# Performance work log

Hardware: AMD Instinct MI355X
Metric: run time of the kernel (lower is better)

The kernel has to match this reference:

```python
import jax, jax.numpy as jnp
import numpy as np
import math

EMB = 1024
HEADS = 16
B, S = 2, 2048


def setup_inputs() -> dict:
    key = jax.random.key(0)
    k_x, k_wq, k_bq, k_wu, k_bu = jax.random.split(key, 5)
    lim = 1.0 / math.sqrt(EMB)
    x = jax.random.normal(k_x, (B, S, EMB), dtype=jnp.float32)
    # nn.Linear weights: [out, in], uniform(-lim, lim)
    wq = jax.random.uniform(k_wq, (EMB, EMB), jnp.float32, -lim, lim)
    bq = jax.random.uniform(k_bq, (EMB,), jnp.float32, -lim, lim)
    wu = jax.random.uniform(k_wu, (EMB, EMB), jnp.float32, -lim, lim)
    bu = jax.random.uniform(k_bu, (EMB,), jnp.float32, -lim, lim)
    return {"x": x, "wq": wq, "bq": bq, "wu": wu, "bu": bu}


def reference(x, wq, bq, wu, bu):
    b, s, emb = x.shape
    hd = emb // HEADS
    # NOTE: faithful to the original bug — Q, K, V all come from toqueries
    q = jnp.einsum('bse,oe->bso', x, wq) + bq  # [B,S,emb]
    # faithful (buggy) reshape: heads in LEADING dim
    qh = q.reshape(HEADS, b, s, hd)
    kh = qh
    vh = qh
    scale = 1.0 / math.sqrt(emb)  # faithful: sqrt(emb), not sqrt(hd)
    scores = jnp.einsum('hbqd,hbkd->hbqk', qh, kh) * scale  # [H,B,S,S]
    attn = jax.nn.softmax(scores, axis=-1)
    out = jnp.einsum('hbqk,hbkd->hbqd', attn, vh)  # [H,B,S,hd]
    out = out.reshape(b, s, emb)
    return jnp.einsum('bse,oe->bso', out, wu) + bu
```

## Files before the change

kernel.cpp:

```cpp
#include <hip/hip_runtime.h>
#include <stdint.h>

#define EMB 1024
#define HEADS 16
#define NB 2
#define NS 2048
#define HD 64
#define NTOK (NB*NS)
#define KVBLK 64
#define QW 32
#define QBLK 128
#define SEXP2 0.04508421676368185f

typedef __attribute__((ext_vector_type(8))) short short8;
typedef __attribute__((ext_vector_type(4))) float f32x4;

__device__ inline unsigned short f2bf(float f) {
  unsigned int x = __builtin_bit_cast(unsigned int, f);
  x += 0x7FFFu + ((x >> 16) & 1u);
  return (unsigned short)(x >> 16);
}

__device__ inline unsigned cvt_pk_bf16(float lo, float hi) {
  unsigned d;
  asm("v_cvt_pk_bf16_f32 %0, %1, %2" : "=v"(d) : "v"(lo), "v"(hi));
  return d;
}

__device__ inline void gld16(const void* g, void* l) {
  __builtin_amdgcn_global_load_lds(
      (const __attribute__((address_space(1))) unsigned int*)g,
      (__attribute__((address_space(3))) unsigned int*)l, 16, 0, 0);
}

__global__ void cvt_bf16_kernel(const float* __restrict__ s,
                                unsigned short* __restrict__ d, int n) {
  int i = (blockIdx.x * blockDim.x + threadIdx.x) * 8;
  if (i >= n) return;
  float4 v0 = *reinterpret_cast<const float4*>(s + i);
  float4 v1 = *reinterpret_cast<const float4*>(s + i + 4);
  short8 o;
  o[0] = (short)f2bf(v0.x); o[1] = (short)f2bf(v0.y);
  o[2] = (short)f2bf(v0.z); o[3] = (short)f2bf(v0.w);
  o[4] = (short)f2bf(v1.x); o[5] = (short)f2bf(v1.y);
  o[6] = (short)f2bf(v1.z); o[7] = (short)f2bf(v1.w);
  *reinterpret_cast<short8*>(d + i) = o;
}

__global__ __launch_bounds__(256) void transpose_kernel(
    const unsigned short* __restrict__ src, unsigned short* __restrict__ dst) {
  __shared__ unsigned short t[64][72];
  const int slab = blockIdx.y, kt = blockIdx.x;
  const unsigned short* s = src + ((size_t)slab * NS + kt * 64) * HD;
  unsigned short* d = dst + (size_t)slab * HD * NS + kt * 64;
  const int tid = threadIdx.x;
  #pragma unroll
  for (int c = 0; c < 2; ++c) {
    int idx = c * 256 + tid;
    int row = idx >> 3, col = (idx & 7) * 8;
    short8 v = *reinterpret_cast<const short8*>(s + row * HD + col);
    *reinterpret_cast<short8*>(&t[row][col]) = v;
  }
  __syncthreads();
  #pragma unroll
  for (int c = 0; c < 2; ++c) {
    int idx = c * 256 + tid;
    int drow = idx >> 3, col = (idx & 7) * 8;
    short8 v;
    #pragma unroll
    for (int j = 0; j < 8; ++j) {
      int p = col + j;
      v[j] = t[(p & 3) * 16 + (p >> 2)][drow];
    }
    *reinterpret_cast<short8*>(d + (size_t)drow * NS + col) = v;
  }
}

template<bool OUT_BF16>
__global__ __launch_bounds__(256) void gemm_bt_kernel(
    const unsigned short* __restrict__ A,
    const unsigned short* __restrict__ Bw,
    const float* __restrict__ bias,
    void* __restrict__ Cout,
    unsigned short* __restrict__ Qscaled,
    int M, int N, int K) {
  __shared__ __align__(16) unsigned short As[2][64 * 64];
  __shared__ __align__(16) unsigned short Bs[2][128 * 64];
  const int tid = threadIdx.x;
  const int lane = tid & 63;
  const int wave = tid >> 6;
  const int wr = wave >> 1, wc = wave & 1;
  const int g = lane >> 4, r = lane & 15;
  const int brow = blockIdx.y * 64;
  const int bcol = blockIdx.x * 128;

  const f32x4 zf = {0.f, 0.f, 0.f, 0.f};
  f32x4 acc[2][4];
  #pragma unroll
  for (int m = 0; m < 2; ++m)
    #pragma unroll
    for (int n = 0; n < 4; ++n) acc[m][n] = zf;

  auto stage = [&](int bb, int k0) {
    #pragma unroll
    for (int i = 0; i < 2; ++i) {
      int base = i * 4096 + wave * 1024;
      int L = base + lane * 16;
      int row = L >> 7, lsl = ((L >> 4) & 7) ^ (row & 7);
      gld16((const char*)A + ((size_t)(brow + row) * K + k0) * 2 + lsl * 16,
            (char*)&As[bb][0] + base);
    }
    #pragma unroll
    for (int i = 0; i < 4; ++i) {
      int base = i * 4096 + wave * 1024;
      int L = base + lane * 16;
      int row = L >> 7, lsl = ((L >> 4) & 7) ^ (row & 7);
      gld16((const char*)Bw + ((size_t)(bcol + row) * K + k0) * 2 + lsl * 16,
            (char*)&Bs[bb][0] + base);
    }
  };

  stage(0, 0);
  int cur = 0;
  for (int k0 = 0; k0 < K; k0 += 64) {
    __syncthreads();
    if (k0 + 64 < K) stage(cur ^ 1, k0 + 64);
    const char* Ac = (const char*)&As[cur][0];
    const char* Bc = (const char*)&Bs[cur][0];
    short8 af[2][2], bfr[4][2];
    #pragma unroll
    for (int m = 0; m < 2; ++m) {
      int row = wr * 32 + m * 16 + r;
      #pragma unroll
      for (int kk = 0; kk < 2; ++kk)
        af[m][kk] = *reinterpret_cast<const short8*>(
            Ac + row * 128 + ((kk * 64 + g * 16) ^ ((row & 7) << 4)));
    }
    #pragma unroll
    for (int n = 0; n < 4; ++n) {
      int row = wc * 64 + n * 16 + r;
      #pragma unroll
      for (int kk = 0; kk < 2; ++kk)
        bfr[n][kk] = *reinterpret_cast<const short8*>(
            Bc + row * 128 + ((kk * 64 + g * 16) ^ ((row & 7) << 4)));
    }
    #pragma unroll
    for (int kk = 0; kk < 2; ++kk)
      #pragma unroll
      for (int m = 0; m < 2; ++m)
        #pragma unroll
        for (int n = 0; n < 4; ++n)
          acc[m][n] = __builtin_amdgcn_mfma_f32_16x16x32_bf16(af[m][kk], bfr[n][kk], acc[m][n], 0, 0, 0);
    cur ^= 1;
  }

  #pragma unroll
  for (int n = 0; n < 4; ++n) {
    int col = bcol + wc * 64 + n * 16 + r;
    float bv = bias[col];
    #pragma unroll
    for (int m = 0; m < 2; ++m) {
      #pragma unroll
      for (int reg = 0; reg < 4; ++reg) {
        int row = brow + wr * 32 + m * 16 + g * 4 + reg;
        float v = acc[m][n][reg] + bv;
        if (OUT_BF16)
          ((unsigned short*)Cout)[(size_t)row * N + col] = f2bf(v);
        else
          ((float*)Cout)[(size_t)row * N + col] = v;
        if (Qscaled)
          Qscaled[(size_t)row * N + col] = f2bf(v * SEXP2);
      }
    }
  }
}

__global__ __launch_bounds__(256) void attn_kernel(
    const unsigned short* __restrict__ qb,
    const unsigned short* __restrict__ qsb,
    const unsigned short* __restrict__ vtb,
    unsigned short* __restrict__ ob) {
  const int slab = blockIdx.y;
  const int qtile = blockIdx.x;
  const unsigned short* Qs = qb + (size_t)slab * NS * HD;
  const unsigned short* Qss = qsb + (size_t)slab * NS * HD;
  const unsigned short* Vts = vtb + (size_t)slab * HD * NS;
  unsigned short* Os = ob + (size_t)slab * NS * HD;
  const int tid = threadIdx.x;
  const int lane = tid & 63;
  const int wave = tid >> 6;
  const int g = lane >> 4, r = lane & 15;
  const int qrow0 = qtile * QBLK + wave * QW;
  const int rkey = (r & 7) << 4;

  __shared__ __align__(16) unsigned short K_lds[2][KVBLK * HD];
  __shared__ __align__(16) unsigned short Vt_lds[2][HD * KVBLK];
  __shared__ __align__(16) unsigned short P_lds[4][QW * KVBLK];
  char* Pb = (char*)&P_lds[wave][0];

  auto stage = [&](int bb, int kt) {
    const char* Kg = (const char*)(Qs + (size_t)kt * KVBLK * HD);
    const char* Vg = (const char*)Vts + (size_t)kt * 128;
    #pragma unroll
    for (int i = 0; i < 2; ++i) {
      int base = i * 4096 + wave * 1024;
      int L = base + lane * 16;
      int row = L >> 7, lsl = ((L >> 4) & 7) ^ (row & 7);
      gld16(Kg + row * 128 + lsl * 16, (char*)&K_lds[bb][0] + base);
      gld16(Vg + (size_t)row * (NS * 2) + lsl * 16, (char*)&Vt_lds[bb][0] + base);
    }
  };

  short8 aq[2][2];
  #pragma unroll
  for (int m = 0; m < 2; ++m)
    #pragma unroll
    for (int kk = 0; kk < 2; ++kk)
      aq[m][kk] = *reinterpret_cast<const short8*>(
          &Qss[(size_t)(qrow0 + m * 16 + r) * HD + kk * 32 + g * 8]);

  const f32x4 zf = {0.f, 0.f, 0.f, 0.f};
  f32x4 o_acc[2][4];
  float l_part[2][4];
  #pragma unroll
  for (int m = 0; m < 2; ++m) {
    #pragma unroll
    for (int n = 0; n < 4; ++n) o_acc[m][n] = zf;
    #pragma unroll
    for (int q = 0; q < 4; ++q) l_part[m][q] = 0.f;
  }

  stage(0, 0);
  int cur = 0;
  for (int kt = 0; kt < NS / KVBLK; ++kt) {
    __syncthreads();
    if (kt + 1 < NS / KVBLK) stage(cur ^ 1, kt + 1);
    const char* Kc = (const char*)&K_lds[cur][0];
    const char* Vc = (const char*)&Vt_lds[cur][0];

    f32x4 s[2][4];
    #pragma unroll
    for (int jb = 0; jb < 4; ++jb) {
      short8 bk[2];
      #pragma unroll
      for (int kk = 0; kk < 2; ++kk)
        bk[kk] = *reinterpret_cast<const short8*>(
            Kc + (jb * 16 + r) * 128 + ((kk * 64 + g * 16) ^ rkey));
      #pragma unroll
      for (int m = 0; m < 2; ++m) {
        s[m][jb] = zf;
        #pragma unroll
        for (int kk = 0; kk < 2; ++kk)
          s[m][jb] = __builtin_amdgcn_mfma_f32_16x16x32_bf16(aq[m][kk], bk[kk], s[m][jb], 0, 0, 0);
      }
    }

    #pragma unroll
    for (int m = 0; m < 2; ++m) {
      #pragma unroll
      for (int reg = 0; reg < 4; ++reg) {
        int prow = m * 16 + g * 4 + reg;
        float p0 = __builtin_amdgcn_exp2f(s[m][0][reg]);
        float p1 = __builtin_amdgcn_exp2f(s[m][1][reg]);
        float p2 = __builtin_amdgcn_exp2f(s[m][2][reg]);
        float p3 = __builtin_amdgcn_exp2f(s[m][3][reg]);
        l_part[m][reg] += (p0 + p1) + (p2 + p3);
        uint2 w;
        w.x = cvt_pk_bf16(p0, p1);
        w.y = cvt_pk_bf16(p2, p3);
        *reinterpret_cast<uint2*>(
            Pb + prow * 128 + ((r * 8) ^ ((prow & 7) << 4))) = w;
      }
    }
    asm volatile("s_waitcnt lgkmcnt(0)" ::: "memory");

    short8 ap[2][2];
    #pragma unroll
    for (int m = 0; m < 2; ++m)
      #pragma unroll
      for (int kk = 0; kk < 2; ++kk)
        ap[m][kk] = *reinterpret_cast<const short8*>(
            Pb + (m * 16 + r) * 128 + ((kk * 64 + g * 16) ^ rkey));
    #pragma unroll
    for (int n = 0; n < 4; ++n) {
      short8 bv[2];
      #pragma unroll
      for (int kk = 0; kk < 2; ++kk)
        bv[kk] = *reinterpret_cast<const short8*>(
            Vc + (n * 16 + r) * 128 + ((kk * 64 + g * 16) ^ rkey));
      #pragma unroll
      for (int m = 0; m < 2; ++m)
        #pragma unroll
        for (int kk = 0; kk < 2; ++kk)
          o_acc[m][n] = __builtin_amdgcn_mfma_f32_16x16x32_bf16(ap[m][kk], bv[kk], o_acc[m][n], 0, 0, 0);
    }
    cur ^= 1;
  }

  #pragma unroll
  for (int m = 0; m < 2; ++m) {
    #pragma unroll
    for (int reg = 0; reg < 4; ++reg) {
      float l = l_part[m][reg];
      #pragma unroll
      for (int off = 1; off < 16; off <<= 1)
        l += __shfl_xor(l, off);
      float inv = 1.f / l;
      int row = qrow0 + m * 16 + g * 4 + reg;
      #pragma unroll
      for (int n = 0; n < 4; ++n)
        Os[(size_t)row * HD + n * 16 + r] = f2bf(o_acc[m][n][reg] * inv);
    }
  }
}

extern "C" void kernel_launch(void* const* d_in, const int* in_sizes, int n_in,
                              void* d_out, int out_size, void* d_ws, size_t ws_size,
                              hipStream_t stream) {
  const float* x  = (const float*)d_in[0];
  const float* wq = (const float*)d_in[1];
  const float* bq = (const float*)d_in[2];
  const float* wu = (const float*)d_in[3];
  const float* bu = (const float*)d_in[4];
  float* out = (float*)d_out;

  char* ws = (char*)d_ws;
  unsigned short* xb  = (unsigned short*)(ws);
  unsigned short* qb  = (unsigned short*)(ws + (8u  << 20));
  unsigned short* ob  = (unsigned short*)(ws + (16u << 20));
  unsigned short* wqb = (unsigned short*)(ws + (24u << 20));
  unsigned short* wub = (unsigned short*)(ws + (26u << 20));

  cvt_bf16_kernel<<<(NTOK * EMB / 8 + 255) / 256, 256, 0, stream>>>(x, xb, NTOK * EMB);
  cvt_bf16_kernel<<<(EMB * EMB / 8 + 255) / 256, 256, 0, stream>>>(wq, wqb, EMB * EMB);
  cvt_bf16_kernel<<<(EMB * EMB / 8 + 255) / 256, 256, 0, stream>>>(wu, wub, EMB * EMB);

  unsigned short* qsb = ob;
  gemm_bt_kernel<true><<<dim3(EMB / 128, NTOK / 64), 256, 0, stream>>>(
      xb, wqb, bq, qb, qsb, NTOK, EMB, EMB);

  unsigned short* vtb = xb;
  transpose_kernel<<<dim3(NS / 64, HEADS * NB), 256, 0, stream>>>(qb, vtb);

  attn_kernel<<<dim3(NS / QBLK, HEADS * NB), 256, 0, stream>>>(qb, qsb, vtb, ob);

  gemm_bt_kernel<false><<<dim3(EMB / 128, NTOK / 64), 256, 0, stream>>>(
      ob, wub, bu, out, (unsigned short*)nullptr, NTOK, EMB, EMB);
}
```

Baseline: 109.2 us.

## Keep softmax probabilities in registers via transposed QK MFMA and XCD-aware grid

Swaps the MFMA operand order for QK^T so each lane holds a transposed score layout. The exponentiated probabilities can then be packed directly into the A-operand registers for the PV MFMA, which removes the per-wave LDS round trip and its waitcnt. The V transpose kernel is re-permuted so the key order matches the new register layout, and the row-sum reduction changes to cross-group shuffles. The attention grid is flattened and remapped so that blocks sharing a slab land on the same XCD, aiming for better L2 reuse of K/V.

```diff
diff --git a/kernel.cpp b/kernel.cpp
--- a/kernel.cpp
+++ b/kernel.cpp
@@ -14,6 +14,7 @@
 
 typedef __attribute__((ext_vector_type(8))) short short8;
 typedef __attribute__((ext_vector_type(4))) float f32x4;
+typedef __attribute__((ext_vector_type(4))) unsigned int u32x4;
 
 __device__ inline unsigned short f2bf(float f) {
   unsigned int x = __builtin_bit_cast(unsigned int, f);
@@ -70,7 +71,8 @@
     #pragma unroll
     for (int j = 0; j < 8; ++j) {
       int p = col + j;
-      v[j] = t[(p & 3) * 16 + (p >> 2)][drow];
+      int kv = (p & 32) | (((p >> 2) & 1) << 4) | (((p >> 3) & 3) << 2) | (p & 3);
+      v[j] = t[kv][drow];
     }
     *reinterpret_cast<short8*>(d + (size_t)drow * NS + col) = v;
   }
@@ -180,8 +182,10 @@
     const unsigned short* __restrict__ qsb,
     const unsigned short* __restrict__ vtb,
     unsigned short* __restrict__ ob) {
-  const int slab = blockIdx.y;
-  const int qtile = blockIdx.x;
+  const int bid = blockIdx.x;
+  const int xcd = bid & 7, idx = bid >> 3;
+  const int slab = xcd * 4 + (idx >> 4);
+  const int qtile = idx & 15;
   const unsigned short* Qs = qb + (size_t)slab * NS * HD;
   const unsigned short* Qss = qsb + (size_t)slab * NS * HD;
   const unsigned short* Vts = vtb + (size_t)slab * HD * NS;
@@ -195,8 +199,6 @@
 
   __shared__ __align__(16) unsigned short K_lds[2][KVBLK * HD];
   __shared__ __align__(16) unsigned short Vt_lds[2][HD * KVBLK];
-  __shared__ __align__(16) unsigned short P_lds[4][QW * KVBLK];
-  char* Pb = (char*)&P_lds[wave][0];
 
   auto stage = [&](int bb, int kt) {
     const char* Kg = (const char*)(Qs + (size_t)kt * KVBLK * HD);
@@ -221,14 +223,11 @@
 
   const f32x4 zf = {0.f, 0.f, 0.f, 0.f};
   f32x4 o_acc[2][4];
-  float l_part[2][4];
-  #pragma unroll
-  for (int m = 0; m < 2; ++m) {
+  float l_lane[2] = {0.f, 0.f};
+  #pragma unroll
+  for (int m = 0; m < 2; ++m)
     #pragma unroll
     for (int n = 0; n < 4; ++n) o_acc[m][n] = zf;
-    #pragma unroll
-    for (int q = 0; q < 4; ++q) l_part[m][q] = 0.f;
-  }
 
   stage(0, 0);
   int cur = 0;
@@ -251,36 +250,35 @@
         s[m][jb] = zf;
         #pragma unroll
         for (int kk = 0; kk < 2; ++kk)
-          s[m][jb] = __builtin_amdgcn_mfma_f32_16x16x32_bf16(aq[m][kk], bk[kk], s[m][jb], 0, 0, 0);
+          s[m][jb] = __builtin_amdgcn_mfma_f32_16x16x32_bf16(bk[kk], aq[m][kk], s[m][jb], 0, 0, 0);
       }
     }
 
+    short8 ap[2][2];
     #pragma unroll
     for (int m = 0; m < 2; ++m) {
-      #pragma unroll
-      for (int reg = 0; reg < 4; ++reg) {
-        int prow = m * 16 + g * 4 + reg;
-        float p0 = __builtin_amdgcn_exp2f(s[m][0][reg]);
-        float p1 = __builtin_amdgcn_exp2f(s[m][1][reg]);
-        float p2 = __builtin_amdgcn_exp2f(s[m][2][reg]);
-        float p3 = __builtin_amdgcn_exp2f(s[m][3][reg]);
-        l_part[m][reg] += (p0 + p1) + (p2 + p3);
-        uint2 w;
-        w.x = cvt_pk_bf16(p0, p1);
-        w.y = cvt_pk_bf16(p2, p3);
-        *reinterpret_cast<uint2*>(
-            Pb + prow * 128 + ((r * 8) ^ ((prow & 7) << 4))) = w;
+      float p[4][4];
+      #pragma unroll
+      for (int jb = 0; jb < 4; ++jb)
+        #pragma unroll
+        for (int reg = 0; reg < 4; ++reg)
+          p[jb][reg] = __builtin_amdgcn_exp2f(s[m][jb][reg]);
+      float t0 = (p[0][0] + p[0][1]) + (p[0][2] + p[0][3]);
+      float t1 = (p[1][0] + p[1][1]) + (p[1][2] + p[1][3]);
+      float t2 = (p[2][0] + p[2][1]) + (p[2][2] + p[2][3]);
+      float t3 = (p[3][0] + p[3][1]) + (p[3][2] + p[3][3]);
+      l_lane[m] += (t0 + t1) + (t2 + t3);
+      #pragma unroll
+      for (int kk = 0; kk < 2; ++kk) {
+        u32x4 w;
+        w.x = cvt_pk_bf16(p[2 * kk][0], p[2 * kk][1]);
+        w.y = cvt_pk_bf16(p[2 * kk][2], p[2 * kk][3]);
+        w.z = cvt_pk_bf16(p[2 * kk + 1][0], p[2 * kk + 1][1]);
+        w.w = cvt_pk_bf16(p[2 * kk + 1][2], p[2 * kk + 1][3]);
+        ap[m][kk] = __builtin_bit_cast(short8, w);
       }
     }
-    asm volatile("s_waitcnt lgkmcnt(0)" ::: "memory");
-
-    short8 ap[2][2];
-    #pragma unroll
-    for (int m = 0; m < 2; ++m)
-      #pragma unroll
-      for (int kk = 0; kk < 2; ++kk)
-        ap[m][kk] = *reinterpret_cast<const short8*>(
-            Pb + (m * 16 + r) * 128 + ((kk * 64 + g * 16) ^ rkey));
+
     #pragma unroll
     for (int n = 0; n < 4; ++n) {
       short8 bv[2];
@@ -299,13 +297,12 @@
 
   #pragma unroll
   for (int m = 0; m < 2; ++m) {
+    float l = l_lane[m];
+    l += __shfl_xor(l, 16);
+    l += __shfl_xor(l, 32);
     #pragma unroll
     for (int reg = 0; reg < 4; ++reg) {
-      float l = l_part[m][reg];
-      #pragma unroll
-      for (int off = 1; off < 16; off <<= 1)
-        l += __shfl_xor(l, off);
-      float inv = 1.f / l;
+      float inv = 1.f / __shfl(l, g * 4 + reg);
       int row = qrow0 + m * 16 + g * 4 + reg;
       #pragma unroll
       for (int n = 0; n < 4; ++n)
@@ -342,7 +339,7 @@
   unsigned short* vtb = xb;
   transpose_kernel<<<dim3(NS / 64, HEADS * NB), 256, 0, stream>>>(qb, vtb);
 
-  attn_kernel<<<dim3(NS / QBLK, HEADS * NB), 256, 0, stream>>>(qb, qsb, vtb, ob);
+  attn_kernel<<<dim3(512), 256, 0, stream>>>(qb, qsb, vtb, ob);
 
   gemm_bt_kernel<false><<<dim3(EMB / 128, NTOK / 64), 256, 0, stream>>>(
       ob, wub, bu, out, (unsigned short*)nullptr, NTOK, EMB, EMB);
```

Result: no change. 108.7 us (-0.5%).
